# Performance work log

Measured on AMD Instinct MI355X. Metric: run time of the kernel, lower is better.

The kernel has to match this reference:

```python
import jax, jax.numpy as jnp
import numpy as np

L = 18                      # tree depth, N = 2**L - 1 nodes (complete binary tree)
N = 2**L - 1               # 262143
D = 128                     # embedding dim
V = 100000                  # vocab size of the single data type
E = 8                       # edge_count


def setup_inputs() -> dict:
    key = jax.random.key(0)
    ks = jax.random.split(key, 8)
    data = jax.random.randint(ks[0], (N,), 0, V)
    edges = jax.random.randint(ks[1], (N,), 0, E)
    data_vecs = jax.random.normal(ks[2], (V, D), dtype=jnp.float32) * 0.1
    # torch uses torch.rand (U[0,1)); scaled for numerical stability over 18 levels
    data_W = jax.random.uniform(ks[3], (D, D), dtype=jnp.float32) * 0.1
    data_b = jax.random.uniform(ks[4], (D,), dtype=jnp.float32) * 0.1
    edge_W = jax.random.uniform(ks[5], (E, D, D), dtype=jnp.float32) * (2.0 / D)
    edge_b = jax.random.uniform(ks[6], (E, D), dtype=jnp.float32) * 0.1
    score_W = jax.random.uniform(ks[7], (D, 1), dtype=jnp.float32)
    return {"data": data, "edges": edges, "data_vecs": data_vecs,
            "data_W": data_W, "data_b": data_b, "edge_W": edge_W,
            "edge_b": edge_b, "score_W": score_W}


def reference(data, edges, data_vecs, data_W, data_b, edge_W, edge_b, score_W):
    # per-node leaf term: addmm(data_bias, data_vecs[data], data_W)  -> [N, D]
    raw = data_vecs[data] @ data_W + data_b
    ret = raw    # value returned to the parent (leaves: unclamped)
    emb = raw    # stored embedding (internal nodes: pre-clamp h)
    # bottom-up over levels; level l occupies indices [2**l - 1, 2**(l+1) - 1)
    for l in reversed(range(L - 1)):
        p0, npar = 2**l - 1, 2**l
        c0, M = 2**(l + 1) - 1, 2**(l + 1)
        child_ret = ret[c0:c0 + M]              # [M, D], siblings adjacent
        eids = edges[c0:c0 + M]                 # [M]
        # edge-weighted child transform: child @ edge_W[e] + edge_b[e]
        contrib = edge_b[eids]
        for e in range(E):                      # small static edge loop
            contrib = contrib + jnp.where((eids == e)[:, None], child_ret, 0.0) @ edge_W[e]
        # sum the two children of each parent, then (leaf + children) / (nc + 1)
        contrib = contrib.reshape(npar, 2, D).sum(axis=1)
        h = (raw[p0:p0 + npar] + contrib) / 3.0
        emb = emb.at[p0:p0 + npar].set(h)
        ret = ret.at[p0:p0 + npar].set(jnp.maximum(h, 0.0))
    scores = (emb @ score_W)[:, 0]              # [N]
    return scores


if __name__ == "__main__":
    out = reference(**setup_inputs())
    print(out.shape, out.dtype)
```

## Files before the change

kernel.cpp:

```cpp
#include <hip/hip_runtime.h>

#define D 128
#define NLVL 17
#define TS 128
#define LVLPAD 1024
#define LDSTR 136
#define LEAF_BLKS 1032
#define CHUNK 2048

typedef float  floatx4 __attribute__((ext_vector_type(4)));
typedef short  shortx8 __attribute__((ext_vector_type(8)));

__device__ __forceinline__ unsigned short f2bf(float f) {
    unsigned u = __float_as_uint(f);
    u += 0x7FFFu + ((u >> 16) & 1u);
    return (unsigned short)(u >> 16);
}
__device__ __forceinline__ float bf2f(unsigned short h) {
    return __uint_as_float(((unsigned)h) << 16);
}
__device__ __forceinline__ int lvl_base_dev(int l) { return ((2 << l) - 2) + LVLPAD * l; }

__global__ __launch_bounds__(256) void count_kernel(
    const int* __restrict__ edges, int* __restrict__ gcnt128, int Nn)
{
    __shared__ int lc[32];
    const int t = threadIdx.x;
    if (t < 32) lc[t] = 0;
    __syncthreads();
    for (int c = 16383 + blockIdx.x * 256 + t; c < Nn; c += gridDim.x * 256) {
        const int e = edges[c];
        const int p = (c - 1) >> 1;
        const int l = 31 - __clz(p + 1);
        atomicAdd(&lc[(l - 13) * 8 + e], 1);
    }
    __syncthreads();
    if (t < 32) gcnt128[blockIdx.x * 32 + t] = lc[t];
}

__global__ __launch_bounds__(256) void prefix_kernel(
    const int* __restrict__ gcnt128, int* __restrict__ gstart,
    int* __restrict__ glim, int* __restrict__ ctr)
{
    __shared__ int part[256];
    __shared__ int tot[32];
    const int t = threadIdx.x;
    const int k = t & 31, bs = t >> 5;
    int s = 0;
    for (int b = bs; b < 128; b += 8) s += gcnt128[b * 32 + k];
    part[t] = s;
    __syncthreads();
    if (t < 32) {
        int tt = 0;
        #pragma unroll
        for (int i = 0; i < 8; i++) tt += part[t + 32 * i];
        tot[t] = tt;
        ctr[t] = 0;
    }
    __syncthreads();
    if (t == 0) {
        for (int li = 0; li < 4; li++) {
            const int l = 13 + li;
            int acc = 0;
            for (int e = 0; e < 8; e++) {
                gstart[l * 9 + e] = acc;
                glim[l * 8 + e] = acc + tot[li * 8 + e];
                acc = (acc + tot[li * 8 + e] + (TS - 1)) & ~(TS - 1);
            }
            gstart[l * 9 + 8] = acc;
        }
    }
}

__global__ __launch_bounds__(256) void place_kernel(
    const int* __restrict__ edges, const int* __restrict__ gstart,
    int* __restrict__ ctr, int* __restrict__ perm, int Nn)
{
    __shared__ unsigned char key_s[CHUNK];
    __shared__ int lcnt[32], lbase[32];
    __shared__ int gs_s[4 * 9];
    const int t = threadIdx.x;
    if (t < 32) lcnt[t] = 0;
    if (t < 36) gs_s[t] = gstart[13 * 9 + t];
    const int base = 16383 + blockIdx.x * CHUNK;
    __syncthreads();
    for (int i = t; i < CHUNK; i += 256) {
        const int c = base + i;
        if (c < Nn) {
            const int e = edges[c];
            const int p = (c - 1) >> 1;
            const int l = 31 - __clz(p + 1);
            const int kk = (l - 13) * 8 + e;
            key_s[i] = (unsigned char)kk;
            atomicAdd(&lcnt[kk], 1);
        } else key_s[i] = 255;
    }
    __syncthreads();
    if (t < 32) {
        const int n = lcnt[t];
        lbase[t] = n ? atomicAdd(&ctr[t], n) : 0;
        lcnt[t] = 0;
    }
    __syncthreads();
    for (int i = t; i < CHUNK; i += 256) {
        const int c = base + i;
        if (c >= Nn) continue;
        const int kk = key_s[i];
        if (kk == 255) continue;
        const int off = atomicAdd(&lcnt[kk], 1);
        const int l = (kk >> 3) + 13, e = kk & 7;
        const int pos = gs_s[(l - 13) * 9 + e] + lbase[kk] + off;
        perm[lvl_base_dev(l) + pos] = c;
    }
}

__global__ __launch_bounds__(256) void prep_kernel(
    const float* __restrict__ dW, const float* __restrict__ db,
    const float* __restrict__ eW, const float* __restrict__ eb,
    const float* __restrict__ sWs, const float* __restrict__ vecs,
    unsigned short* __restrict__ ewt, unsigned short* __restrict__ cwt,
    unsigned short* __restrict__ dwt, float* __restrict__ dcomp,
    float* __restrict__ sv, float* __restrict__ s0,
    unsigned short* __restrict__ vbf, int n4)
{
    __shared__ float smem[8448];
    const int b = blockIdx.x, t = threadIdx.x;
    if (b < 32) {
        float* w_s = smem;
        float* cs  = smem + 4096;
        const int e = b >> 2, cc = b & 3;
        for (int i = t; i < D * 8; i += 256) {
            const int k = i >> 3, j4 = i & 7;
            ((float4*)w_s)[i] = ((const float4*)eW)[((size_t)e * D + k) * 32 + cc * 8 + j4];
        }
        __syncthreads();
        const int r2 = t >> 1, h = t & 1;
        float4 acc[4];
        #pragma unroll
        for (int m = 0; m < 4; m++) acc[m] = make_float4(0.f, 0.f, 0.f, 0.f);
        for (int k = 0; k < D; k++) {
            const float a = dW[(size_t)r2 * D + k];
            #pragma unroll
            for (int m = 0; m < 4; m++) {
                const float4 w4 = ((const float4*)w_s)[k * 8 + h * 4 + m];
                acc[m].x += a * w4.x; acc[m].y += a * w4.y; acc[m].z += a * w4.z; acc[m].w += a * w4.w;
            }
        }
        #pragma unroll
        for (int m = 0; m < 4; m++) {
            cs[r2 * 33 + h * 16 + m * 4 + 0] = acc[m].x;
            cs[r2 * 33 + h * 16 + m * 4 + 1] = acc[m].y;
            cs[r2 * 33 + h * 16 + m * 4 + 2] = acc[m].z;
            cs[r2 * 33 + h * 16 + m * 4 + 3] = acc[m].w;
        }
        __syncthreads();
        {
            const int nn = t >> 3, kseg = t & 7, k0 = kseg * 16;
            unsigned ow[8];
            #pragma unroll
            for (int i2 = 0; i2 < 8; i2++) {
                const unsigned short lo = f2bf(cs[(k0 + 2 * i2) * 33 + nn]);
                const unsigned short hi = f2bf(cs[(k0 + 2 * i2 + 1) * 33 + nn]);
                ow[i2] = (unsigned)lo | ((unsigned)hi << 16);
            }
            uint4* dstp = (uint4*)(cwt + (size_t)e * D * D + (size_t)(cc * 32 + nn) * D + k0);
            dstp[0] = make_uint4(ow[0], ow[1], ow[2], ow[3]);
            dstp[1] = make_uint4(ow[4], ow[5], ow[6], ow[7]);
        }
        if (t < 32) {
            float a2 = 0.f;
            for (int k = 0; k < D; k++) a2 += db[k] * w_s[k * 32 + t];
            dcomp[e * D + cc * 32 + t] = a2 + eb[e * D + cc * 32 + t];
        }
    } else if (b < 41) {
        float* lds = smem;
        const int bb = b - 32;
        const float* src = (bb < 8) ? (eW + (size_t)bb * D * D) : dW;
        unsigned short* dst = (bb < 8) ? (ewt + (size_t)bb * D * D) : dwt;
        for (int half = 0; half < 2; half++) {
            __syncthreads();
            for (int i = t; i < 64 * D / 4; i += 256) {
                float4 v = ((const float4*)src)[half * (64 * D / 4) + i];
                const int k = (i * 4) >> 7, n = (i * 4) & 127;
                lds[k * 129 + n]     = v.x;
                lds[k * 129 + n + 1] = v.y;
                lds[k * 129 + n + 2] = v.z;
                lds[k * 129 + n + 3] = v.w;
            }
            __syncthreads();
            const int n = t >> 1, hh = t & 1;
            for (int kk = 0; kk < 32; kk++) {
                const int k = hh * 32 + kk;
                dst[(size_t)n * D + half * 64 + k] = f2bf(lds[k * 129 + n]);
            }
        }
    } else if (b == 41) {
        float* red = smem;
        if (t < D) {
            float acc = 0.f;
            for (int j = 0; j < D; j++) acc += dW[(size_t)t * D + j] * sWs[j];
            sv[t] = acc;
        }
        red[t] = (t < D) ? db[t] * sWs[t] : 0.f;
        __syncthreads();
        for (int s = 128; s > 0; s >>= 1) { if (t < s) red[t] += red[t + s]; __syncthreads(); }
        if (t == 0) s0[0] = red[0];
    } else {
        for (int i = (b - 42) * 256 + t; i < n4; i += (gridDim.x - 42) * 256) {
            const float4 v = ((const float4*)vecs)[i];
            uint2 o;
            o.x = (unsigned)f2bf(v.x) | ((unsigned)f2bf(v.y) << 16);
            o.y = (unsigned)f2bf(v.z) | ((unsigned)f2bf(v.w) << 16);
            ((uint2*)vbf)[i] = o;
        }
    }
}

__global__ __launch_bounds__(256, 4) void leaf_embed_kernel(
    unsigned short* __restrict__ X,
    const unsigned short* __restrict__ vbf,
    const int* __restrict__ data,
    const int* __restrict__ perm,
    const int* __restrict__ gstart9,
    const int* __restrict__ glim8,
    const unsigned short* __restrict__ cwt,
    const float* __restrict__ dcomp,
    const float* __restrict__ sv, const float* __restrict__ s0p,
    const unsigned short* __restrict__ dwt,
    const float* __restrict__ db,
    float* __restrict__ out,
    int NI, int lbase_leaf)
{
    __shared__ unsigned short a_s[TS * LDSTR];
    const int t = threadIdx.x;
    const bool is_leaf = (blockIdx.x < LEAF_BLKS);
    const int r = t >> 1, h = t & 1;

    int e = 0, c;
    const unsigned short* Wg;
    const float* bias;
    if (is_leaf) {
        const int ts = blockIdx.x * TS;
        if (ts >= gstart9[8]) return;
        #pragma unroll
        for (int j = 1; j < 8; j++) if (ts >= gstart9[j]) e = j;
        const int p = ts + r;
        c = (p < glim8[e]) ? perm[lbase_leaf + p] : -1;
        Wg = cwt + (size_t)e * D * D;
        bias = dcomp + (size_t)e * D;
    } else {
        const int node = (blockIdx.x - LEAF_BLKS) * TS + r;
        c = (node < NI) ? node : -1;
        Wg = dwt;
        bias = db;
    }

    {
        unsigned short* dst = a_s + r * LDSTR + h * 64;
        if (c >= 0) {
            const uint4* src = (const uint4*)(vbf + (size_t)data[c] * D + h * 64);
            if (is_leaf) {
                float sc = 0.f;
                #pragma unroll
                for (int j = 0; j < 8; j++) {
                    const uint4 v = src[j];
                    const unsigned* pv = (const unsigned*)&v;
                    #pragma unroll
                    for (int u = 0; u < 4; u++) {
                        const int n = h * 64 + j * 8 + u * 2;
                        sc += bf2f((unsigned short)pv[u]) * sv[n]
                            + bf2f((unsigned short)(pv[u] >> 16)) * sv[n + 1];
                    }
                    ((uint4*)dst)[j] = v;
                }
                sc += __shfl_xor(sc, 1, 64);
                if (h == 0) out[c] = sc + s0p[0];
            } else {
                #pragma unroll
                for (int j = 0; j < 8; j++) ((uint4*)dst)[j] = src[j];
            }
        } else {
            #pragma unroll
            for (int j = 0; j < 8; j++) ((uint4*)dst)[j] = make_uint4(0u, 0u, 0u, 0u);
        }
    }
    __syncthreads();

    const int lane = t & 63, wv = t >> 6;
    const int cq = lane & 15, q = lane >> 4;
    const floatx4 z4 = {0.f, 0.f, 0.f, 0.f};
    floatx4 acc[8][2];
    #pragma unroll
    for (int i = 0; i < 8; i++) { acc[i][0] = z4; acc[i][1] = z4; }
    #pragma unroll
    for (int ks = 0; ks < 4; ks++) {
        shortx8 bfr[2];
        #pragma unroll
        for (int nl = 0; nl < 2; nl++) {
            const int n = (wv * 2 + nl) * 16 + cq;
            bfr[nl] = *(const shortx8*)(Wg + (size_t)n * D + ks * 32 + q * 8);
        }
        #pragma unroll
        for (int mt = 0; mt < 8; mt++) {
            const shortx8 af = *(const shortx8*)(a_s + (mt * 16 + cq) * LDSTR + ks * 32 + q * 8);
            acc[mt][0] = __builtin_amdgcn_mfma_f32_16x16x32_bf16(af, bfr[0], acc[mt][0], 0, 0, 0);
            acc[mt][1] = __builtin_amdgcn_mfma_f32_16x16x32_bf16(af, bfr[1], acc[mt][1], 0, 0, 0);
        }
    }
    __syncthreads();
    #pragma unroll
    for (int nl = 0; nl < 2; nl++) {
        const int n = (wv * 2 + nl) * 16 + cq;
        const float bn = bias[n];
        #pragma unroll
        for (int mt = 0; mt < 8; mt++) {
            #pragma unroll
            for (int rg = 0; rg < 4; rg++) {
                const int m = mt * 16 + q * 4 + rg;
                a_s[m * LDSTR + n] = f2bf(acc[mt][nl][rg] + bn);
            }
        }
    }
    __syncthreads();
    if (c >= 0) {
        uint4* dst = (uint4*)(X + (size_t)c * D + h * 64);
        const uint4* srcl = (const uint4*)(a_s + r * LDSTR + h * 64);
        #pragma unroll
        for (int j = 0; j < 8; j++) dst[j] = srcl[j];
    }
}

__global__ __launch_bounds__(256, 4) void tree_gemm_kernel(
    unsigned short* __restrict__ X,
    const int* __restrict__ perm,
    const int* __restrict__ gstart9,
    const int* __restrict__ glim8,
    const unsigned short* __restrict__ ewt,
    const float* __restrict__ eb,
    const float* __restrict__ svec,
    float* __restrict__ out,
    int lbase)
{
    __shared__ unsigned short a_s[TS * LDSTR];
    const int t = threadIdx.x;
    const int ts = blockIdx.x * TS;
    if (ts >= gstart9[8]) return;
    int e = 0;
    #pragma unroll
    for (int j = 1; j < 8; j++) if (ts >= gstart9[j]) e = j;
    const int r = t >> 1, h = t & 1;
    const int p = ts + r;
    const int c = (p < glim8[e]) ? perm[lbase + p] : -1;
    const unsigned short* Wg = ewt + (size_t)e * D * D;

    {
        unsigned short* dst = a_s + r * LDSTR + h * 64;
        if (c >= 0) {
            const uint4* xr = (const uint4*)(X + (size_t)c * D + h * 64);
            const uint4* ya = (const uint4*)(X + (size_t)(2 * c + 1) * D + h * 64);
            const uint4* yb = (const uint4*)(X + (size_t)(2 * c + 2) * D + h * 64);
            const float inv3 = 1.0f / 3.0f;
            float sc = 0.f;
            #pragma unroll
            for (int j = 0; j < 8; j++) {
                uint4 ra = xr[j], rb = ya[j], rc = yb[j];
                const unsigned* pa = (const unsigned*)&ra;
                const unsigned* pb = (const unsigned*)&rb;
                const unsigned* pc = (const unsigned*)&rc;
                unsigned ou[4];
                #pragma unroll
                for (int u = 0; u < 4; u++) {
                    const float h0 = (bf2f((unsigned short)pa[u]) + bf2f((unsigned short)pb[u])
                                    + bf2f((unsigned short)pc[u])) * inv3;
                    const float h1 = (bf2f((unsigned short)(pa[u] >> 16)) + bf2f((unsigned short)(pb[u] >> 16))
                                    + bf2f((unsigned short)(pc[u] >> 16))) * inv3;
                    const int n = h * 64 + j * 8 + u * 2;
                    sc += h0 * svec[n] + h1 * svec[n + 1];
                    unsigned short q0 = f2bf(h0), q1 = f2bf(h1);
                    q0 = (q0 & 0x8000u) ? 0 : q0;
                    q1 = (q1 & 0x8000u) ? 0 : q1;
                    ou[u] = (unsigned)q0 | ((unsigned)q1 << 16);
                }
                ((uint4*)dst)[j] = make_uint4(ou[0], ou[1], ou[2], ou[3]);
            }
            sc += __shfl_xor(sc, 1, 64);
            if (h == 0) out[c] = sc;
        } else {
            #pragma unroll
            for (int j = 0; j < 8; j++) ((uint4*)dst)[j] = make_uint4(0u, 0u, 0u, 0u);
        }
    }
    __syncthreads();
    const int lane = t & 63, wv = t >> 6;
    const int cq = lane & 15, q = lane >> 4;
    const floatx4 z4 = {0.f, 0.f, 0.f, 0.f};
    floatx4 acc[8][2];
    #pragma unroll
    for (int i = 0; i < 8; i++) { acc[i][0] = z4; acc[i][1] = z4; }
    #pragma unroll
    for (int ks = 0; ks < 4; ks++) {
        shortx8 bfr[2];
        #pragma unroll
        for (int nl = 0; nl < 2; nl++) {
            const int n = (wv * 2 + nl) * 16 + cq;
            bfr[nl] = *(const shortx8*)(Wg + (size_t)n * D + ks * 32 + q * 8);
        }
        #pragma unroll
        for (int mt = 0; mt < 8; mt++) {
            const shortx8 af = *(const shortx8*)(a_s + (mt * 16 + cq) * LDSTR + ks * 32 + q * 8);
            acc[mt][0] = __builtin_amdgcn_mfma_f32_16x16x32_bf16(af, bfr[0], acc[mt][0], 0, 0, 0);
            acc[mt][1] = __builtin_amdgcn_mfma_f32_16x16x32_bf16(af, bfr[1], acc[mt][1], 0, 0, 0);
        }
    }
    __syncthreads();
    #pragma unroll
    for (int nl = 0; nl < 2; nl++) {
        const int n = (wv * 2 + nl) * 16 + cq;
        const float bn = eb[(size_t)e * D + n];
        #pragma unroll
        for (int mt = 0; mt < 8; mt++) {
            #pragma unroll
            for (int rg = 0; rg < 4; rg++) {
                const int m = mt * 16 + q * 4 + rg;
                a_s[m * LDSTR + n] = f2bf(acc[mt][nl][rg] + bn);
            }
        }
    }
    __syncthreads();
    if (c >= 0) {
        uint4* dst = (uint4*)(X + (size_t)c * D + h * 64);
        const uint4* srcl = (const uint4*)(a_s + r * LDSTR + h * 64);
        #pragma unroll
        for (int j = 0; j < 8; j++) dst[j] = srcl[j];
    }
}

__global__ __launch_bounds__(256) void sub_kernel(
    unsigned short* __restrict__ X,
    const float* __restrict__ eW,
    const float* __restrict__ eb,
    const int* __restrict__ edges,
    const float* __restrict__ sW,
    float* __restrict__ out,
    int rbase, int nlev)
{
    __shared__ __align__(16) float xbuf[4][D];
    const int t = threadIdx.x, wv = t >> 6, lane = t & 63;
    const int u = rbase + blockIdx.x;
    const int j2 = lane * 2;
    const float inv3 = 1.0f / 3.0f;

    for (int lev = nlev - 1; lev >= 0; lev--) {
        const int first = ((u + 1) << lev) - 1;
        const int cnt = 1 << lev;
        for (int i = wv; i < cnt; i += 4) {
            const int n = first + i;
            const unsigned ra = *(const unsigned*)(X + (size_t)n * D + j2);
            const unsigned rb = *(const unsigned*)(X + (size_t)(2 * n + 1) * D + j2);
            const unsigned rc = *(const unsigned*)(X + (size_t)(2 * n + 2) * D + j2);
            const float h0 = (bf2f((unsigned short)ra) + bf2f((unsigned short)rb)
                            + bf2f((unsigned short)rc)) * inv3;
            const float h1 = (bf2f((unsigned short)(ra >> 16)) + bf2f((unsigned short)(rb >> 16))
                            + bf2f((unsigned short)(rc >> 16))) * inv3;
            float sc = h0 * sW[j2] + h1 * sW[j2 + 1];
            #pragma unroll
            for (int o = 32; o > 0; o >>= 1) sc += __shfl_xor(sc, o, 64);
            if (lane == 0) out[n] = sc;
            if (n == 0) continue;
            float2 x2 = make_float2(fmaxf(h0, 0.f), fmaxf(h1, 0.f));
            *(float2*)(xbuf[wv] + j2) = x2;
            const int e = edges[n];
            const float* W = eW + (size_t)e * D * D;
            float y0 = 0.f, y1 = 0.f;
            #pragma unroll 8
            for (int k4 = 0; k4 < 32; k4++) {
                const float4 xk = *(const float4*)(xbuf[wv] + k4 * 4);
                const float2 w0 = *(const float2*)(W + (size_t)(k4 * 4 + 0) * D + j2);
                const float2 w1 = *(const float2*)(W + (size_t)(k4 * 4 + 1) * D + j2);
                const float2 w2 = *(const float2*)(W + (size_t)(k4 * 4 + 2) * D + j2);
                const float2 w3 = *(const float2*)(W + (size_t)(k4 * 4 + 3) * D + j2);
                y0 += xk.x * w0.x + xk.y * w1.x + xk.z * w2.x + xk.w * w3.x;
                y1 += xk.x * w0.y + xk.y * w1.y + xk.z * w2.y + xk.w * w3.y;
            }
            y0 += eb[e * D + j2];
            y1 += eb[e * D + j2 + 1];
            const unsigned o = (unsigned)f2bf(y0) | ((unsigned)f2bf(y1) << 16);
            *(unsigned*)(X + (size_t)n * D + j2) = o;
        }
        __syncthreads();
    }
}

extern "C" void kernel_launch(void* const* d_in, const int* in_sizes, int n_in,
                              void* d_out, int out_size, void* d_ws, size_t ws_size,
                              hipStream_t stream) {
    const int*   data      = (const int*)d_in[0];
    const int*   edges     = (const int*)d_in[1];
    const float* data_vecs = (const float*)d_in[2];
    const float* data_W    = (const float*)d_in[3];
    const float* data_b    = (const float*)d_in[4];
    const float* edge_W    = (const float*)d_in[5];
    const float* edge_b    = (const float*)d_in[6];
    const float* score_W   = (const float*)d_in[7];
    float* out = (float*)d_out;

    const int Nn = in_sizes[0];
    const int NI = Nn >> 1;
    const int VD = in_sizes[2];
    const int PERM_TOTAL = (Nn - 1) + LVLPAD * NLVL;

    char* w = (char*)d_ws;
    size_t off = 0;
    unsigned short* X = (unsigned short*)(w + off); off += (size_t)Nn * D * 2;
    int* perm = (int*)(w + off);  off += (size_t)PERM_TOTAL * 4;
    off = (off + 255) & ~(size_t)255;
    int* gstart  = (int*)(w + off); off += NLVL * 9 * 4;
    int* glim    = (int*)(w + off); off += NLVL * 8 * 4;
    int* gcnt128 = (int*)(w + off); off += 128 * 32 * 4;
    int* ctr     = (int*)(w + off); off += 32 * 4;
    off = (off + 255) & ~(size_t)255;
    float* dcomp = (float*)(w + off); off += 8 * D * 4;
    float* sv    = (float*)(w + off); off += D * 4;
    float* s0    = (float*)(w + off); off += 256;
    off = (off + 255) & ~(size_t)255;
    unsigned short* ewt = (unsigned short*)(w + off); off += (size_t)8 * D * D * 2;
    unsigned short* cwt = (unsigned short*)(w + off); off += (size_t)8 * D * D * 2;
    unsigned short* dwt = (unsigned short*)(w + off); off += (size_t)D * D * 2;
    off = (off + 255) & ~(size_t)255;
    unsigned short* vbf = (unsigned short*)(w + off); off += (size_t)VD * 2;

    count_kernel<<<128, 256, 0, stream>>>(edges, gcnt128, Nn);
    prefix_kernel<<<1, 256, 0, stream>>>(gcnt128, gstart, glim, ctr);
    const int place_blks = (Nn - 16383 + CHUNK - 1) / CHUNK;
    place_kernel<<<place_blks, 256, 0, stream>>>(edges, gstart, ctr, perm, Nn);

    prep_kernel<<<42 + 1024, 256, 0, stream>>>(
        data_W, data_b, edge_W, edge_b, score_W, data_vecs,
        ewt, cwt, dwt, dcomp, sv, s0, vbf, VD / 4);

    {
        const int embed_blks = (NI + TS - 1) / TS;
        const int lbase_leaf = ((2 << 16) - 2) + LVLPAD * 16;
        leaf_embed_kernel<<<LEAF_BLKS + embed_blks, 256, 0, stream>>>(
            X, vbf, data, perm, gstart + 16 * 9, glim + 16 * 8,
            cwt, dcomp, sv, s0, dwt, data_b, out, NI, lbase_leaf);
    }

    for (int l = 15; l >= 13; l--) {
        const int M = 2 << l;
        const int lbase = ((2 << l) - 2) + LVLPAD * l;
        tree_gemm_kernel<<<M / TS + 8, 256, 0, stream>>>(
            X, perm, gstart + l * 9, glim + l * 8, ewt, edge_b, score_W, out, lbase);
    }

    sub_kernel<<<2048, 256, 0, stream>>>(X, edge_W, edge_b, edges, score_W, out, 2047, 3);
    sub_kernel<<<128, 256, 0, stream>>>(X, edge_W, edge_b, edges, score_W, out, 127, 4);
    sub_kernel<<<8, 256, 0, stream>>>(X, edge_W, edge_b, edges, score_W, out, 7, 4);
    sub_kernel<<<1, 256, 0, stream>>>(X, edge_W, edge_b, edges, score_W, out, 0, 3);
}
```

Before: 339.4 us.

## Fuse counting into prep, prefix into place, restructure leaf GEMM, bf16 sub weights

```diff
diff --git a/kernel.cpp b/kernel.cpp
--- a/kernel.cpp
+++ b/kernel.cpp
@@ -7,6 +7,7 @@
 #define LDSTR 136
 #define LEAF_BLKS 1032
 #define CHUNK 2048
+#define CNT_BLKS 128
 
 typedef float  floatx4 __attribute__((ext_vector_type(4)));
 typedef short  shortx8 __attribute__((ext_vector_type(8)));
@@ -21,106 +22,15 @@
 }
 __device__ __forceinline__ int lvl_base_dev(int l) { return ((2 << l) - 2) + LVLPAD * l; }
 
-__global__ __launch_bounds__(256) void count_kernel(
-    const int* __restrict__ edges, int* __restrict__ gcnt128, int Nn)
-{
-    __shared__ int lc[32];
-    const int t = threadIdx.x;
-    if (t < 32) lc[t] = 0;
-    __syncthreads();
-    for (int c = 16383 + blockIdx.x * 256 + t; c < Nn; c += gridDim.x * 256) {
-        const int e = edges[c];
-        const int p = (c - 1) >> 1;
-        const int l = 31 - __clz(p + 1);
-        atomicAdd(&lc[(l - 13) * 8 + e], 1);
-    }
-    __syncthreads();
-    if (t < 32) gcnt128[blockIdx.x * 32 + t] = lc[t];
-}
-
-__global__ __launch_bounds__(256) void prefix_kernel(
-    const int* __restrict__ gcnt128, int* __restrict__ gstart,
-    int* __restrict__ glim, int* __restrict__ ctr)
-{
-    __shared__ int part[256];
-    __shared__ int tot[32];
-    const int t = threadIdx.x;
-    const int k = t & 31, bs = t >> 5;
-    int s = 0;
-    for (int b = bs; b < 128; b += 8) s += gcnt128[b * 32 + k];
-    part[t] = s;
-    __syncthreads();
-    if (t < 32) {
-        int tt = 0;
-        #pragma unroll
-        for (int i = 0; i < 8; i++) tt += part[t + 32 * i];
-        tot[t] = tt;
-        ctr[t] = 0;
-    }
-    __syncthreads();
-    if (t == 0) {
-        for (int li = 0; li < 4; li++) {
-            const int l = 13 + li;
-            int acc = 0;
-            for (int e = 0; e < 8; e++) {
-                gstart[l * 9 + e] = acc;
-                glim[l * 8 + e] = acc + tot[li * 8 + e];
-                acc = (acc + tot[li * 8 + e] + (TS - 1)) & ~(TS - 1);
-            }
-            gstart[l * 9 + 8] = acc;
-        }
-    }
-}
-
-__global__ __launch_bounds__(256) void place_kernel(
-    const int* __restrict__ edges, const int* __restrict__ gstart,
-    int* __restrict__ ctr, int* __restrict__ perm, int Nn)
-{
-    __shared__ unsigned char key_s[CHUNK];
-    __shared__ int lcnt[32], lbase[32];
-    __shared__ int gs_s[4 * 9];
-    const int t = threadIdx.x;
-    if (t < 32) lcnt[t] = 0;
-    if (t < 36) gs_s[t] = gstart[13 * 9 + t];
-    const int base = 16383 + blockIdx.x * CHUNK;
-    __syncthreads();
-    for (int i = t; i < CHUNK; i += 256) {
-        const int c = base + i;
-        if (c < Nn) {
-            const int e = edges[c];
-            const int p = (c - 1) >> 1;
-            const int l = 31 - __clz(p + 1);
-            const int kk = (l - 13) * 8 + e;
-            key_s[i] = (unsigned char)kk;
-            atomicAdd(&lcnt[kk], 1);
-        } else key_s[i] = 255;
-    }
-    __syncthreads();
-    if (t < 32) {
-        const int n = lcnt[t];
-        lbase[t] = n ? atomicAdd(&ctr[t], n) : 0;
-        lcnt[t] = 0;
-    }
-    __syncthreads();
-    for (int i = t; i < CHUNK; i += 256) {
-        const int c = base + i;
-        if (c >= Nn) continue;
-        const int kk = key_s[i];
-        if (kk == 255) continue;
-        const int off = atomicAdd(&lcnt[kk], 1);
-        const int l = (kk >> 3) + 13, e = kk & 7;
-        const int pos = gs_s[(l - 13) * 9 + e] + lbase[kk] + off;
-        perm[lvl_base_dev(l) + pos] = c;
-    }
-}
-
 __global__ __launch_bounds__(256) void prep_kernel(
     const float* __restrict__ dW, const float* __restrict__ db,
     const float* __restrict__ eW, const float* __restrict__ eb,
     const float* __restrict__ sWs, const float* __restrict__ vecs,
+    const int* __restrict__ edges,
     unsigned short* __restrict__ ewt, unsigned short* __restrict__ cwt,
     unsigned short* __restrict__ dwt, float* __restrict__ dcomp,
-    float* __restrict__ sv, float* __restrict__ s0,
+    float* __restrict__ sv, float* __restrict__ s0, int* __restrict__ ctr,
+    int* __restrict__ gcnt128, int Nn,
     unsigned short* __restrict__ vbf, int n4)
 {
     __shared__ float smem[8448];
@@ -196,6 +106,7 @@
         }
     } else if (b == 41) {
         float* red = smem;
+        if (t < 32) ctr[t] = 0;
         if (t < D) {
             float acc = 0.f;
             for (int j = 0; j < D; j++) acc += dW[(size_t)t * D + j] * sWs[j];
@@ -205,14 +116,99 @@
         __syncthreads();
         for (int s = 128; s > 0; s >>= 1) { if (t < s) red[t] += red[t + s]; __syncthreads(); }
         if (t == 0) s0[0] = red[0];
+    } else if (b < 42 + CNT_BLKS) {
+        int* lc = (int*)smem;
+        if (t < 32) lc[t] = 0;
+        __syncthreads();
+        for (int c = 16383 + (b - 42) * 256 + t; c < Nn; c += CNT_BLKS * 256) {
+            const int e = edges[c];
+            const int p = (c - 1) >> 1;
+            const int l = 31 - __clz(p + 1);
+            atomicAdd(&lc[(l - 13) * 8 + e], 1);
+        }
+        __syncthreads();
+        if (t < 32) gcnt128[(b - 42) * 32 + t] = lc[t];
     } else {
-        for (int i = (b - 42) * 256 + t; i < n4; i += (gridDim.x - 42) * 256) {
+        for (int i = (b - 42 - CNT_BLKS) * 256 + t; i < n4; i += (gridDim.x - 42 - CNT_BLKS) * 256) {
             const float4 v = ((const float4*)vecs)[i];
             uint2 o;
             o.x = (unsigned)f2bf(v.x) | ((unsigned)f2bf(v.y) << 16);
             o.y = (unsigned)f2bf(v.z) | ((unsigned)f2bf(v.w) << 16);
             ((uint2*)vbf)[i] = o;
         }
+    }
+}
+
+__global__ __launch_bounds__(256) void place_kernel(
+    const int* __restrict__ edges, const int* __restrict__ gcnt128,
+    int* __restrict__ gstart, int* __restrict__ glim,
+    int* __restrict__ ctr, int* __restrict__ perm, int Nn)
+{
+    __shared__ unsigned char key_s[CHUNK];
+    __shared__ int part[256];
+    __shared__ int tot[32];
+    __shared__ int lcnt[32], lbase[32];
+    __shared__ int gs_s[4 * 9], gl_s[32];
+    const int t = threadIdx.x;
+    {
+        const int k = t & 31, bs = t >> 5;
+        int s = 0;
+        for (int bb = bs; bb < CNT_BLKS; bb += 8) s += gcnt128[bb * 32 + k];
+        part[t] = s;
+    }
+    if (t < 32) lcnt[t] = 0;
+    __syncthreads();
+    if (t < 32) {
+        int tt = 0;
+        #pragma unroll
+        for (int i = 0; i < 8; i++) tt += part[t + 32 * i];
+        tot[t] = tt;
+    }
+    __syncthreads();
+    if (t == 0) {
+        for (int li = 0; li < 4; li++) {
+            int acc = 0;
+            for (int e = 0; e < 8; e++) {
+                gs_s[li * 9 + e] = acc;
+                gl_s[li * 8 + e] = acc + tot[li * 8 + e];
+                acc = (acc + tot[li * 8 + e] + (TS - 1)) & ~(TS - 1);
+            }
+            gs_s[li * 9 + 8] = acc;
+        }
+    }
+    __syncthreads();
+    if (blockIdx.x == 0 && t < 36) {
+        gstart[13 * 9 + t] = gs_s[t];
+        if (t < 32) glim[13 * 8 + t] = gl_s[t];
+    }
+    const int base = 16383 + blockIdx.x * CHUNK;
+    for (int i = t; i < CHUNK; i += 256) {
+        const int c = base + i;
+        if (c < Nn) {
+            const int e = edges[c];
+            const int p = (c - 1) >> 1;
+            const int l = 31 - __clz(p + 1);
+            const int kk = (l - 13) * 8 + e;
+            key_s[i] = (unsigned char)kk;
+            atomicAdd(&lcnt[kk], 1);
+        } else key_s[i] = 255;
+    }
+    __syncthreads();
+    if (t < 32) {
+        const int n = lcnt[t];
+        lbase[t] = n ? atomicAdd(&ctr[t], n) : 0;
+        lcnt[t] = 0;
+    }
+    __syncthreads();
+    for (int i = t; i < CHUNK; i += 256) {
+        const int c = base + i;
+        if (c >= Nn) continue;
+        const int kk = key_s[i];
+        if (kk == 255) continue;
+        const int off = atomicAdd(&lcnt[kk], 1);
+        const int l = (kk >> 3) + 13, e = kk & 7;
+        const int pos = gs_s[(l - 13) * 9 + e] + lbase[kk] + off;
+        perm[lvl_base_dev(l) + pos] = c;
     }
 }
 
@@ -231,100 +227,101 @@
     float* __restrict__ out,
     int NI, int lbase_leaf)
 {
-    __shared__ unsigned short a_s[TS * LDSTR];
+    __shared__ unsigned short y_s[4][32 * LDSTR];
+    __shared__ int crow[128];
     const int t = threadIdx.x;
+    const int lane = t & 63, wv = t >> 6;
+    const int cq = lane & 15, q = lane >> 4;
     const bool is_leaf = (blockIdx.x < LEAF_BLKS);
-    const int r = t >> 1, h = t & 1;
-
-    int e = 0, c;
+
+    int e = 0, ts;
     const unsigned short* Wg;
     const float* bias;
     if (is_leaf) {
-        const int ts = blockIdx.x * TS;
+        ts = blockIdx.x * TS;
         if (ts >= gstart9[8]) return;
         #pragma unroll
         for (int j = 1; j < 8; j++) if (ts >= gstart9[j]) e = j;
-        const int p = ts + r;
-        c = (p < glim8[e]) ? perm[lbase_leaf + p] : -1;
         Wg = cwt + (size_t)e * D * D;
         bias = dcomp + (size_t)e * D;
     } else {
-        const int node = (blockIdx.x - LEAF_BLKS) * TS + r;
-        c = (node < NI) ? node : -1;
+        ts = (blockIdx.x - LEAF_BLKS) * TS;
         Wg = dwt;
         bias = db;
     }
 
-    {
-        unsigned short* dst = a_s + r * LDSTR + h * 64;
-        if (c >= 0) {
-            const uint4* src = (const uint4*)(vbf + (size_t)data[c] * D + h * 64);
-            if (is_leaf) {
-                float sc = 0.f;
-                #pragma unroll
-                for (int j = 0; j < 8; j++) {
-                    const uint4 v = src[j];
-                    const unsigned* pv = (const unsigned*)&v;
-                    #pragma unroll
-                    for (int u = 0; u < 4; u++) {
-                        const int n = h * 64 + j * 8 + u * 2;
-                        sc += bf2f((unsigned short)pv[u]) * sv[n]
-                            + bf2f((unsigned short)(pv[u] >> 16)) * sv[n + 1];
-                    }
-                    ((uint4*)dst)[j] = v;
-                }
-                sc += __shfl_xor(sc, 1, 64);
-                if (h == 0) out[c] = sc + s0p[0];
-            } else {
-                #pragma unroll
-                for (int j = 0; j < 8; j++) ((uint4*)dst)[j] = src[j];
-            }
+    int c[2];
+    const unsigned short* arow[2];
+    #pragma unroll
+    for (int mti = 0; mti < 2; mti++) {
+        const int rl = wv * 32 + mti * 16 + cq;
+        int cc;
+        if (is_leaf) {
+            const int p = ts + rl;
+            cc = (p < glim8[e]) ? perm[lbase_leaf + p] : -1;
         } else {
-            #pragma unroll
-            for (int j = 0; j < 8; j++) ((uint4*)dst)[j] = make_uint4(0u, 0u, 0u, 0u);
-        }
-    }
-    __syncthreads();
-
-    const int lane = t & 63, wv = t >> 6;
-    const int cq = lane & 15, q = lane >> 4;
+            const int node = ts + rl;
+            cc = (node < NI) ? node : -1;
+        }
+        c[mti] = cc;
+        arow[mti] = (cc >= 0) ? (vbf + (size_t)data[cc] * D) : (const unsigned short*)0;
+        if (q == 0) crow[rl] = cc;
+    }
+
     const floatx4 z4 = {0.f, 0.f, 0.f, 0.f};
-    floatx4 acc[8][2];
-    #pragma unroll
-    for (int i = 0; i < 8; i++) { acc[i][0] = z4; acc[i][1] = z4; }
+    floatx4 acc[2][8];
+    #pragma unroll
+    for (int i = 0; i < 8; i++) { acc[0][i] = z4; acc[1][i] = z4; }
+    float sc0 = 0.f, sc1 = 0.f;
+
     #pragma unroll
     for (int ks = 0; ks < 4; ks++) {
-        shortx8 bfr[2];
-        #pragma unroll
-        for (int nl = 0; nl < 2; nl++) {
-            const int n = (wv * 2 + nl) * 16 + cq;
-            bfr[nl] = *(const shortx8*)(Wg + (size_t)n * D + ks * 32 + q * 8);
-        }
-        #pragma unroll
-        for (int mt = 0; mt < 8; mt++) {
-            const shortx8 af = *(const shortx8*)(a_s + (mt * 16 + cq) * LDSTR + ks * 32 + q * 8);
-            acc[mt][0] = __builtin_amdgcn_mfma_f32_16x16x32_bf16(af, bfr[0], acc[mt][0], 0, 0, 0);
-            acc[mt][1] = __builtin_amdgcn_mfma_f32_16x16x32_bf16(af, bfr[1], acc[mt][1], 0, 0, 0);
-        }
-    }
-    __syncthreads();
-    #pragma unroll
-    for (int nl = 0; nl < 2; nl++) {
-        const int n = (wv * 2 + nl) * 16 + cq;
+        shortx8 af[2];
+        #pragma unroll
+        for (int mti = 0; mti < 2; mti++) {
+            if (c[mti] >= 0) af[mti] = *(const shortx8*)(arow[mti] + ks * 32 + q * 8);
+            else { shortx8 z = {0,0,0,0,0,0,0,0}; af[mti] = z; }
+        }
+        if (is_leaf) {
+            #pragma unroll
+            for (int j = 0; j < 8; j++) {
+                const float svj = sv[ks * 32 + q * 8 + j];
+                sc0 += bf2f((unsigned short)af[0][j]) * svj;
+                sc1 += bf2f((unsigned short)af[1][j]) * svj;
+            }
+        }
+        #pragma unroll
+        for (int nt = 0; nt < 8; nt++) {
+            const shortx8 bfr = *(const shortx8*)(Wg + (size_t)(nt * 16 + cq) * D + ks * 32 + q * 8);
+            acc[0][nt] = __builtin_amdgcn_mfma_f32_16x16x32_bf16(af[0], bfr, acc[0][nt], 0, 0, 0);
+            acc[1][nt] = __builtin_amdgcn_mfma_f32_16x16x32_bf16(af[1], bfr, acc[1][nt], 0, 0, 0);
+        }
+    }
+    if (is_leaf) {
+        sc0 += __shfl_xor(sc0, 16, 64); sc0 += __shfl_xor(sc0, 32, 64);
+        sc1 += __shfl_xor(sc1, 16, 64); sc1 += __shfl_xor(sc1, 32, 64);
+        if (q == 0) {
+            if (c[0] >= 0) out[c[0]] = sc0 + s0p[0];
+            if (c[1] >= 0) out[c[1]] = sc1 + s0p[0];
+        }
+    }
+    unsigned short* ys = y_s[wv];
+    #pragma unroll
+    for (int nt = 0; nt < 8; nt++) {
+        const int n = nt * 16 + cq;
         const float bn = bias[n];
         #pragma unroll
-        for (int mt = 0; mt < 8; mt++) {
-            #pragma unroll
-            for (int rg = 0; rg < 4; rg++) {
-                const int m = mt * 16 + q * 4 + rg;
-                a_s[m * LDSTR + n] = f2bf(acc[mt][nl][rg] + bn);
-            }
-        }
-    }
-    __syncthreads();
-    if (c >= 0) {
-        uint4* dst = (uint4*)(X + (size_t)c * D + h * 64);
-        const uint4* srcl = (const uint4*)(a_s + r * LDSTR + h * 64);
+        for (int mti = 0; mti < 2; mti++) {
+            #pragma unroll
+            for (int rg = 0; rg < 4; rg++)
+                ys[(mti * 16 + q * 4 + rg) * LDSTR + n] = f2bf(acc[mti][nt][rg] + bn);
+        }
+    }
+    const int r2 = lane >> 1, h = lane & 1;
+    const int cc = crow[wv * 32 + r2];
+    if (cc >= 0) {
+        uint4* dst = (uint4*)(X + (size_t)cc * D + h * 64);
+        const uint4* srcl = (const uint4*)(ys + r2 * LDSTR + h * 64);
         #pragma unroll
         for (int j = 0; j < 8; j++) dst[j] = srcl[j];
     }
@@ -437,7 +434,7 @@
 
 __global__ __launch_bounds__(256) void sub_kernel(
     unsigned short* __restrict__ X,
-    const float* __restrict__ eW,
+    const unsigned short* __restrict__ ewt,
     const float* __restrict__ eb,
     const int* __restrict__ edges,
     const float* __restrict__ sW,
@@ -470,17 +467,22 @@
             float2 x2 = make_float2(fmaxf(h0, 0.f), fmaxf(h1, 0.f));
             *(float2*)(xbuf[wv] + j2) = x2;
             const int e = edges[n];
-            const float* W = eW + (size_t)e * D * D;
+            const unsigned short* W0 = ewt + (size_t)e * D * D + (size_t)j2 * D;
             float y0 = 0.f, y1 = 0.f;
-            #pragma unroll 8
-            for (int k4 = 0; k4 < 32; k4++) {
-                const float4 xk = *(const float4*)(xbuf[wv] + k4 * 4);
-                const float2 w0 = *(const float2*)(W + (size_t)(k4 * 4 + 0) * D + j2);
-                const float2 w1 = *(const float2*)(W + (size_t)(k4 * 4 + 1) * D + j2);
-                const float2 w2 = *(const float2*)(W + (size_t)(k4 * 4 + 2) * D + j2);
-                const float2 w3 = *(const float2*)(W + (size_t)(k4 * 4 + 3) * D + j2);
-                y0 += xk.x * w0.x + xk.y * w1.x + xk.z * w2.x + xk.w * w3.x;
-                y1 += xk.x * w0.y + xk.y * w1.y + xk.z * w2.y + xk.w * w3.y;
+            #pragma unroll 4
+            for (int k8 = 0; k8 < 16; k8++) {
+                const uint4 wa = *(const uint4*)(W0 + k8 * 8);
+                const uint4 wb = *(const uint4*)(W0 + D + k8 * 8);
+                const float4 xa = *(const float4*)(xbuf[wv] + k8 * 8);
+                const float4 xb = *(const float4*)(xbuf[wv] + k8 * 8 + 4);
+                y0 += bf2f((unsigned short)wa.x) * xa.x + bf2f((unsigned short)(wa.x >> 16)) * xa.y
+                    + bf2f((unsigned short)wa.y) * xa.z + bf2f((unsigned short)(wa.y >> 16)) * xa.w
+                    + bf2f((unsigned short)wa.z) * xb.x + bf2f((unsigned short)(wa.z >> 16)) * xb.y
+                    + bf2f((unsigned short)wa.w) * xb.z + bf2f((unsigned short)(wa.w >> 16)) * xb.w;
+                y1 += bf2f((unsigned short)wb.x) * xa.x + bf2f((unsigned short)(wb.x >> 16)) * xa.y
+                    + bf2f((unsigned short)wb.y) * xa.z + bf2f((unsigned short)(wb.y >> 16)) * xa.w
+                    + bf2f((unsigned short)wb.z) * xb.x + bf2f((unsigned short)(wb.z >> 16)) * xb.y
+                    + bf2f((unsigned short)wb.w) * xb.z + bf2f((unsigned short)(wb.w >> 16)) * xb.w;
             }
             y0 += eb[e * D + j2];
             y1 += eb[e * D + j2 + 1];
@@ -516,7 +518,7 @@
     off = (off + 255) & ~(size_t)255;
     int* gstart  = (int*)(w + off); off += NLVL * 9 * 4;
     int* glim    = (int*)(w + off); off += NLVL * 8 * 4;
-    int* gcnt128 = (int*)(w + off); off += 128 * 32 * 4;
+    int* gcnt128 = (int*)(w + off); off += CNT_BLKS * 32 * 4;
     int* ctr     = (int*)(w + off); off += 32 * 4;
     off = (off + 255) & ~(size_t)255;
     float* dcomp = (float*)(w + off); off += 8 * D * 4;
@@ -529,14 +531,12 @@
     off = (off + 255) & ~(size_t)255;
     unsigned short* vbf = (unsigned short*)(w + off); off += (size_t)VD * 2;
 
-    count_kernel<<<128, 256, 0, stream>>>(edges, gcnt128, Nn);
-    prefix_kernel<<<1, 256, 0, stream>>>(gcnt128, gstart, glim, ctr);
+    prep_kernel<<<42 + CNT_BLKS + 1024, 256, 0, stream>>>(
+        data_W, data_b, edge_W, edge_b, score_W, data_vecs, edges,
+        ewt, cwt, dwt, dcomp, sv, s0, ctr, gcnt128, Nn, vbf, VD / 4);
+
     const int place_blks = (Nn - 16383 + CHUNK - 1) / CHUNK;
-    place_kernel<<<place_blks, 256, 0, stream>>>(edges, gstart, ctr, perm, Nn);
-
-    prep_kernel<<<42 + 1024, 256, 0, stream>>>(
-        data_W, data_b, edge_W, edge_b, score_W, data_vecs,
-        ewt, cwt, dwt, dcomp, sv, s0, vbf, VD / 4);
+    place_kernel<<<place_blks, 256, 0, stream>>>(edges, gcnt128, gstart, glim, ctr, perm, Nn);
 
     {
         const int embed_blks = (NI + TS - 1) / TS;
@@ -553,8 +553,8 @@
             X, perm, gstart + l * 9, glim + l * 8, ewt, edge_b, score_W, out, lbase);
     }
 
-    sub_kernel<<<2048, 256, 0, stream>>>(X, edge_W, edge_b, edges, score_W, out, 2047, 3);
-    sub_kernel<<<128, 256, 0, stream>>>(X, edge_W, edge_b, edges, score_W, out, 127, 4);
-    sub_kernel<<<8, 256, 0, stream>>>(X, edge_W, edge_b, edges, score_W, out, 7, 4);
-    sub_kernel<<<1, 256, 0, stream>>>(X, edge_W, edge_b, edges, score_W, out, 0, 3);
-}
+    sub_kernel<<<2048, 256, 0, stream>>>(X, ewt, edge_b, edges, score_W, out, 2047, 3);
+    sub_kernel<<<128, 256, 0, stream>>>(X, ewt, edge_b, edges, score_W, out, 127, 4);
+    sub_kernel<<<8, 256, 0, stream>>>(X, ewt, edge_b, edges, score_W, out, 7, 4);
+    sub_kernel<<<1, 256, 0, stream>>>(X, ewt, edge_b, edges, score_W, out, 0, 3);
+}
```

Result: slower. 369.5 us (+8.9%).
